# Kernel optimization log

Hardware: AMD Instinct MI355X
Metric: run time of the kernel (lower is better)

Reference implementation:

```python
import jax, jax.numpy as jnp
import numpy as np
import math

B, S, CIN, H, W = 8, 8, 64, 32, 32
COUT, K = 128, 3
PW = COUT * CIN * K * K  # 73728
P = PW + COUT            # 73856


def setup_inputs() -> dict:
    key = jax.random.key(0)
    ks = jax.random.split(key, 6)
    return {
        "x": jax.random.normal(ks[0], (B, S, CIN, H, W), dtype=jnp.float32),
        "e": jax.random.normal(ks[1], (S, P), dtype=jnp.float32),
        "mu_w": jax.random.normal(ks[2], (PW,), dtype=jnp.float32) * 0.02,
        "rho_w": jax.random.normal(ks[3], (PW,), dtype=jnp.float32) * 0.5,
        "mu_b": jax.random.normal(ks[4], (COUT,), dtype=jnp.float32) * 0.02,
        "rho_b": jax.random.normal(ks[5], (COUT,), dtype=jnp.float32) * 0.5,
    }


def _unit_log_mfg(v):
    # v: [s_n, D]; -log(2*pi)*D/2 - sum(v**2)/2  (scalar, matching torch code)
    two_pi = jnp.asarray(2.0 * math.pi, v.dtype)
    return -jnp.log(two_pi) * (v.shape[1] / 2.0) - jnp.sum(v * v) / 2.0


def reference(x, e, mu_w, rho_w, mu_b, rho_b):
    s_n = e.shape[0]
    cout = mu_b.shape[0]
    cin = x.shape[2]
    k = int(round(math.sqrt(mu_w.shape[0] / (cout * cin))))
    pw = mu_w.shape[0]

    sig_w = jax.nn.softplus(rho_w)  # log(1+exp(rho))
    sig_b = jax.nn.softplus(rho_b)
    w = mu_w[None, :] + sig_w[None, :] * e[:, :pw]          # [s_n, PW]
    b = mu_b[None, :] + sig_b[None, :] * e[:, pw:pw + cout]  # [s_n, COUT]

    entropy_q = jnp.sum(jnp.log(sig_w)) + jnp.sum(jnp.log(sig_b))
    cross_entropy_qp = _unit_log_mfg(w) + _unit_log_mfg(b)
    kl_qp = -entropy_q - cross_entropy_qp

    w5 = w.reshape(s_n, cout, cin, k, k)  # per-sample OIHW kernels

    # per-sample conv: vmap over the sample axis j; batch conv over data axis i
    def conv_one(xj, wj):  # xj [B,CIN,H,W], wj [COUT,CIN,K,K]
        return jax.lax.conv(xj, wj, (1, 1), 'VALID')

    out = jax.vmap(conv_one, in_axes=(1, 0), out_axes=1)(x, w5)  # [B,S,COUT,H',W']
    out = out + b[None, :, :, None, None]
    return out, kl_qp
```

## Files before the change

kernel.cpp:

```cpp
#include <hip/hip_runtime.h>
#include <hip/hip_bf16.h>
#include <math.h>

#define Bn    8
#define Sn    8
#define COUTc 128
#define PWc   73728
#define Pc    73856
#define WOc   30
#define NPIX  900
#define GPIX  7200
#define NSTEP 9
#define TILE  128
#define NT2   57

typedef __bf16 bf16;
typedef bf16  bf16x8 __attribute__((ext_vector_type(8)));
typedef float f32x16 __attribute__((ext_vector_type(16)));

__device__ __forceinline__ float softplus_f(float x) {
    return fmaxf(x, 0.f) + log1pf(expf(-fabsf(x)));
}

__device__ __forceinline__ unsigned int pack2(float a, float b) {
    unsigned short ua = __builtin_bit_cast(unsigned short, (bf16)a);
    unsigned short ub = __builtin_bit_cast(unsigned short, (bf16)b);
    return ((unsigned int)ub << 16) | (unsigned int)ua;
}

__device__ __forceinline__ void gl16(const void* g, void* l) {
    typedef __attribute__((address_space(1))) void gvoid;
    typedef __attribute__((address_space(3))) void lvoid;
    __builtin_amdgcn_global_load_lds((gvoid*)g, (lvoid*)l, 16, 0, 0);
}

__global__ __launch_bounds__(256) void prep_all(
        const float* __restrict__ xg, const float* __restrict__ e,
        const float* __restrict__ mu_w, const float* __restrict__ rho_w,
        const float* __restrict__ mu_b, const float* __restrict__ rho_b,
        bf16* __restrict__ xt, bf16* __restrict__ wimg,
        float* __restrict__ bq, float* __restrict__ slots) {
    const int bid = blockIdx.x;
    const int t   = threadIdx.x;

    if (bid < 512) {
        const int img  = bid >> 3;
        const int part = bid & 7;
        const int p    = part * 128 + (t >> 1);
        const int half = t & 1;
        const float* src = xg + ((size_t)img << 16) + (size_t)(half * 32) * 1024 + p;
        bf16*        dst = xt + ((size_t)img << 16) + (size_t)p * 64 + half * 32;
        #pragma unroll
        for (int o = 0; o < 4; ++o) {
            uint4 pk;
            pk.x = pack2(src[(o * 8 + 0) * 1024], src[(o * 8 + 1) * 1024]);
            pk.y = pack2(src[(o * 8 + 2) * 1024], src[(o * 8 + 3) * 1024]);
            pk.z = pack2(src[(o * 8 + 4) * 1024], src[(o * 8 + 5) * 1024]);
            pk.w = pack2(src[(o * 8 + 6) * 1024], src[(o * 8 + 7) * 1024]);
            *reinterpret_cast<uint4*>(dst + o * 8) = pk;
        }
        return;
    }

    float ls = 0.f, sq = 0.f;
    if (bid < 544) {
        const int gidx = (bid - 512) * 256 + t;
        const int co   = gidx >> 6;
        const int ci   = gidx & 63;
        const int p0   = co * 576 + ci * 9;
        float mu[9], sg[9];
        #pragma unroll
        for (int r = 0; r < 9; ++r) {
            mu[r] = mu_w[p0 + r];
            sg[r] = softplus_f(rho_w[p0 + r]);
            ls   += logf(sg[r]);
        }
        const int dstp = (co << 6) + (((ci >> 3) ^ (co & 7)) << 3) + (ci & 7);
        #pragma unroll
        for (int s = 0; s < Sn; ++s) {
            const float* es = e + s * Pc + p0;
            #pragma unroll
            for (int r = 0; r < 9; ++r) {
                float wv = fmaf(sg[r], es[r], mu[r]);
                wimg[((s * NSTEP + r) << 13) + dstp] = (bf16)wv;
                sq += wv * wv;
            }
        }
    } else {
        if (t < COUTc) {
            float sig = softplus_f(rho_b[t]);
            ls = logf(sig);
            float mu = mu_b[t];
            #pragma unroll
            for (int s = 0; s < Sn; ++s) {
                float bv = fmaf(sig, e[s * Pc + PWc + t], mu);
                bq[s * COUTc + t] = bv;
                sq += bv * bv;
            }
        }
    }

    #pragma unroll
    for (int off = 32; off > 0; off >>= 1) {
        ls += __shfl_down(ls, off);
        sq += __shfl_down(sq, off);
    }
    __shared__ float sls[4], ssq[4];
    const int lane = t & 63, wd = t >> 6;
    if (lane == 0) { sls[wd] = ls; ssq[wd] = sq; }
    __syncthreads();
    if (t == 0) {
        slots[2 * (bid - 512)]     = sls[0] + sls[1] + sls[2] + sls[3];
        slots[2 * (bid - 512) + 1] = ssq[0] + ssq[1] + ssq[2] + ssq[3];
    }
}

__global__ __launch_bounds__(128) void conv_mfma(
        const bf16* __restrict__ xt, const bf16* __restrict__ wimg,
        const float* __restrict__ bq, const float* __restrict__ slots,
        float* __restrict__ out, float* __restrict__ klout) {
    const int bid  = blockIdx.x;
    const int s    = bid & 7;
    const int tile = bid >> 3;
    const int t    = threadIdx.x;
    const int lane = t & 63;
    const int w    = t >> 6;

    __shared__ bf16 Wbuf[2][8192];
    __shared__ bf16 Xbuf[2][8192];

    const char* wsrcL = (const char*)wimg + ((size_t)(s * NSTEP) << 14)
                      + (w << 13) + (lane << 4);

    const char* xs[8];
    #pragma unroll
    for (int q = 0; q < 8; ++q) {
        int pix = w * 64 + q * 8 + (lane >> 3);
        int g   = tile * TILE + pix;
        if (g >= GPIX) g = GPIX - 1;
        int b2 = g / NPIX;
        int rr = g - b2 * NPIX;
        int oy = rr / WOc;
        int ox = rr - oy * WOc;
        int m  = (lane & 7) ^ (pix & 7);
        xs[q] = (const char*)xt
            + ((((size_t)(b2 * Sn + s) << 10) + oy * 32 + ox) << 7) + (m << 4);
    }

    f32x16 acc[2][4];
    #pragma unroll
    for (int i = 0; i < 2; ++i)
        #pragma unroll
        for (int j = 0; j < 4; ++j)
            #pragma unroll
            for (int k = 0; k < 16; ++k)
                acc[i][j][k] = 0.f;

    #define STAGE(stepc, b)                                                  \
    {                                                                        \
        const char* ws_ = wsrcL + ((stepc) << 14);                           \
        char* wl_ = (char*)(&Wbuf[(b)][0]) + (w << 13);                      \
        _Pragma("unroll")                                                    \
        for (int q = 0; q < 8; ++q)                                          \
            gl16(ws_ + (q << 10), wl_ + (q << 10));                          \
        const int roff_ = (((stepc) / 3) * 32 + ((stepc) % 3)) * 128;        \
        char* xl_ = (char*)(&Xbuf[(b)][0]) + (w << 13);                      \
        _Pragma("unroll")                                                    \
        for (int q = 0; q < 8; ++q)                                          \
            gl16(xs[q] + roff_, xl_ + (q << 10));                            \
    }

    #define COMPUTE(b)                                                       \
    {                                                                        \
        const bf16* Wl_ = &Wbuf[(b)][0];                                     \
        const bf16* Xl_ = &Xbuf[(b)][0];                                     \
        _Pragma("unroll")                                                    \
        for (int kc = 0; kc < 4; ++kc) {                                     \
            const int oct_ = ((kc << 1) + (lane >> 5)) ^ (lane & 7);         \
            bf16x8 a0 = *reinterpret_cast<const bf16x8*>(                    \
                Wl_ + ((w * 64 + (lane & 31)) << 6) + (oct_ << 3));          \
            bf16x8 a1 = *reinterpret_cast<const bf16x8*>(                    \
                Wl_ + ((w * 64 + 32 + (lane & 31)) << 6) + (oct_ << 3));     \
            bf16x8 b0 = *reinterpret_cast<const bf16x8*>(                    \
                Xl_ + (((lane & 31)) << 6) + (oct_ << 3));                   \
            bf16x8 b1 = *reinterpret_cast<const bf16x8*>(                    \
                Xl_ + ((32 + (lane & 31)) << 6) + (oct_ << 3));              \
            bf16x8 b2 = *reinterpret_cast<const bf16x8*>(                    \
                Xl_ + ((64 + (lane & 31)) << 6) + (oct_ << 3));              \
            bf16x8 b3 = *reinterpret_cast<const bf16x8*>(                    \
                Xl_ + ((96 + (lane & 31)) << 6) + (oct_ << 3));              \
            acc[0][0] = __builtin_amdgcn_mfma_f32_32x32x16_bf16(a0, b0, acc[0][0], 0, 0, 0); \
            acc[0][1] = __builtin_amdgcn_mfma_f32_32x32x16_bf16(a0, b1, acc[0][1], 0, 0, 0); \
            acc[0][2] = __builtin_amdgcn_mfma_f32_32x32x16_bf16(a0, b2, acc[0][2], 0, 0, 0); \
            acc[0][3] = __builtin_amdgcn_mfma_f32_32x32x16_bf16(a0, b3, acc[0][3], 0, 0, 0); \
            acc[1][0] = __builtin_amdgcn_mfma_f32_32x32x16_bf16(a1, b0, acc[1][0], 0, 0, 0); \
            acc[1][1] = __builtin_amdgcn_mfma_f32_32x32x16_bf16(a1, b1, acc[1][1], 0, 0, 0); \
            acc[1][2] = __builtin_amdgcn_mfma_f32_32x32x16_bf16(a1, b2, acc[1][2], 0, 0, 0); \
            acc[1][3] = __builtin_amdgcn_mfma_f32_32x32x16_bf16(a1, b3, acc[1][3], 0, 0, 0); \
        }                                                                    \
    }

    STAGE(0, 0);
    STAGE(1, 1);

    #define ITER(tt, b)                                                      \
        asm volatile("s_waitcnt vmcnt(16)" ::: "memory");                    \
        __builtin_amdgcn_s_barrier();                                        \
        __builtin_amdgcn_sched_barrier(0);                                   \
        COMPUTE(b);                                                          \
        __builtin_amdgcn_sched_barrier(0);                                   \
        __builtin_amdgcn_s_barrier();                                        \
        STAGE((tt) + 2, b);

    ITER(0, 0)
    ITER(1, 1)
    ITER(2, 0)
    ITER(3, 1)
    ITER(4, 0)
    ITER(5, 1)
    ITER(6, 0)
    asm volatile("s_waitcnt vmcnt(16)" ::: "memory");
    __builtin_amdgcn_s_barrier();
    __builtin_amdgcn_sched_barrier(0);
    COMPUTE(1);
    asm volatile("s_waitcnt vmcnt(0)" ::: "memory");
    __builtin_amdgcn_s_barrier();
    __builtin_amdgcn_sched_barrier(0);
    COMPUTE(0);

    #undef ITER
    #undef COMPUTE
    #undef STAGE

    const int colp = lane & 31;
    const int hi   = lane >> 5;
    #pragma unroll
    for (int i = 0; i < 2; ++i) {
        float bs[16];
        #pragma unroll
        for (int reg = 0; reg < 16; ++reg) {
            int co = w * 64 + i * 32 + (reg & 3) + 8 * (reg >> 2) + 4 * hi;
            bs[reg] = bq[s * COUTc + co];
        }
        #pragma unroll
        for (int j = 0; j < 4; ++j) {
            int gg = tile * TILE + j * 32 + colp;
            if (gg >= GPIX) continue;
            int b2 = gg / NPIX;
            int r2 = gg - b2 * NPIX;
            float* ob = out + (size_t)(b2 * Sn + s) * (COUTc * NPIX) + r2;
            #pragma unroll
            for (int reg = 0; reg < 16; ++reg) {
                int co = w * 64 + i * 32 + (reg & 3) + 8 * (reg >> 2) + 4 * hi;
                ob[co * NPIX] = acc[i][j][reg] + bs[reg];
            }
        }
    }

    if (bid == 0 && w == 0) {
        float ls = 0.f, sq = 0.f;
        for (int i = lane; i < 33; i += 64) {
            ls += slots[2 * i];
            sq += slots[2 * i + 1];
        }
        #pragma unroll
        for (int off = 32; off > 0; off >>= 1) {
            ls += __shfl_down(ls, off);
            sq += __shfl_down(sq, off);
        }
        if (lane == 0)
            *klout = -ls + 0.91893853320467274f * (float)Pc + 0.5f * sq;
    }
}

extern "C" void kernel_launch(void* const* d_in, const int* in_sizes, int n_in,
                              void* d_out, int out_size, void* d_ws, size_t ws_size,
                              hipStream_t stream) {
    const float* x     = (const float*)d_in[0];
    const float* e     = (const float*)d_in[1];
    const float* mu_w  = (const float*)d_in[2];
    const float* rho_w = (const float*)d_in[3];
    const float* mu_b  = (const float*)d_in[4];
    const float* rho_b = (const float*)d_in[5];
    float* out = (float*)d_out;

    bf16*  wimg  = (bf16*)d_ws;
    float* bq    = (float*)((char*)d_ws + 1179648);
    float* slots = (float*)((char*)d_ws + 1183744);
    bf16*  xt    = (bf16*)((char*)d_ws + 1187840);

    prep_all<<<dim3(545), dim3(256), 0, stream>>>(
        x, e, mu_w, rho_w, mu_b, rho_b, xt, wimg, bq, slots);

    conv_mfma<<<dim3(NT2 * Sn), dim3(128), 0, stream>>>(
        xt, wimg, bq, slots, out, out + (out_size - 1));
}
```

Measured before the change: 35.17 us.

## Replace LDS-staged MFMA conv with direct-global-load single-wave tiles

Drops the double-buffered LDS staging with global_load_lds and barriers. Instead, each 64-thread block computes a 64-cout by 64-pixel tile and loads MFMA operands straight from global memory into registers. The weight and activation workspace layouts are changed to channel-octet-major so each lane's 16-byte fragment is read directly. Running many more small blocks (1808) is meant to raise occupancy and remove sync overhead, at the cost of less data reuse per block and more L2 traffic.

Measured after the change: 40.98 us. 16.5% more time.

```diff
diff --git a/kernel.cpp b/kernel.cpp
--- a/kernel.cpp
+++ b/kernel.cpp
@@ -11,8 +11,6 @@
 #define NPIX  900
 #define GPIX  7200
 #define NSTEP 9
-#define TILE  128
-#define NT2   57
 
 typedef __bf16 bf16;
 typedef bf16  bf16x8 __attribute__((ext_vector_type(8)));
@@ -28,17 +26,11 @@
     return ((unsigned int)ub << 16) | (unsigned int)ua;
 }
 
-__device__ __forceinline__ void gl16(const void* g, void* l) {
-    typedef __attribute__((address_space(1))) void gvoid;
-    typedef __attribute__((address_space(3))) void lvoid;
-    __builtin_amdgcn_global_load_lds((gvoid*)g, (lvoid*)l, 16, 0, 0);
-}
-
 __global__ __launch_bounds__(256) void prep_all(
         const float* __restrict__ xg, const float* __restrict__ e,
         const float* __restrict__ mu_w, const float* __restrict__ rho_w,
         const float* __restrict__ mu_b, const float* __restrict__ rho_b,
-        bf16* __restrict__ xt, bf16* __restrict__ wimg,
+        bf16* __restrict__ xt, bf16* __restrict__ wq,
         float* __restrict__ bq, float* __restrict__ slots) {
     const int bid = blockIdx.x;
     const int t   = threadIdx.x;
@@ -46,10 +38,9 @@
     if (bid < 512) {
         const int img  = bid >> 3;
         const int part = bid & 7;
-        const int p    = part * 128 + (t >> 1);
-        const int half = t & 1;
+        const int p    = part * 128 + (t & 127);
+        const int half = t >> 7;
         const float* src = xg + ((size_t)img << 16) + (size_t)(half * 32) * 1024 + p;
-        bf16*        dst = xt + ((size_t)img << 16) + (size_t)p * 64 + half * 32;
         #pragma unroll
         for (int o = 0; o < 4; ++o) {
             uint4 pk;
@@ -57,7 +48,8 @@
             pk.y = pack2(src[(o * 8 + 2) * 1024], src[(o * 8 + 3) * 1024]);
             pk.z = pack2(src[(o * 8 + 4) * 1024], src[(o * 8 + 5) * 1024]);
             pk.w = pack2(src[(o * 8 + 6) * 1024], src[(o * 8 + 7) * 1024]);
-            *reinterpret_cast<uint4*>(dst + o * 8) = pk;
+            size_t idx16 = ((size_t)(img * 8 + half * 4 + o) << 10) + p;
+            *reinterpret_cast<uint4*>(xt + (idx16 << 3)) = pk;
         }
         return;
     }
@@ -75,14 +67,14 @@
             sg[r] = softplus_f(rho_w[p0 + r]);
             ls   += logf(sg[r]);
         }
-        const int dstp = (co << 6) + (((ci >> 3) ^ (co & 7)) << 3) + (ci & 7);
+        const int dstp = ((((ci >> 3) << 7) + co) << 3) + (ci & 7);
         #pragma unroll
         for (int s = 0; s < Sn; ++s) {
             const float* es = e + s * Pc + p0;
             #pragma unroll
             for (int r = 0; r < 9; ++r) {
                 float wv = fmaf(sg[r], es[r], mu[r]);
-                wimg[((s * NSTEP + r) << 13) + dstp] = (bf16)wv;
+                wq[(((s * NSTEP + r) << 10) << 3) + dstp] = (bf16)wv;
                 sq += wv * wv;
             }
         }
@@ -115,161 +107,89 @@
     }
 }
 
-__global__ __launch_bounds__(128) void conv_mfma(
-        const bf16* __restrict__ xt, const bf16* __restrict__ wimg,
+__global__ __launch_bounds__(64) void conv_mfma(
+        const bf16* __restrict__ xt, const bf16* __restrict__ wq,
         const float* __restrict__ bq, const float* __restrict__ slots,
         float* __restrict__ out, float* __restrict__ klout) {
     const int bid  = blockIdx.x;
     const int s    = bid & 7;
-    const int tile = bid >> 3;
-    const int t    = threadIdx.x;
-    const int lane = t & 63;
-    const int w    = t >> 6;
-
-    __shared__ bf16 Wbuf[2][8192];
-    __shared__ bf16 Xbuf[2][8192];
-
-    const char* wsrcL = (const char*)wimg + ((size_t)(s * NSTEP) << 14)
-                      + (w << 13) + (lane << 4);
-
-    const char* xs[8];
-    #pragma unroll
-    for (int q = 0; q < 8; ++q) {
-        int pix = w * 64 + q * 8 + (lane >> 3);
-        int g   = tile * TILE + pix;
-        if (g >= GPIX) g = GPIX - 1;
-        int b2 = g / NPIX;
-        int rr = g - b2 * NPIX;
-        int oy = rr / WOc;
-        int ox = rr - oy * WOc;
-        int m  = (lane & 7) ^ (pix & 7);
-        xs[q] = (const char*)xt
-            + ((((size_t)(b2 * Sn + s) << 10) + oy * 32 + ox) << 7) + (m << 4);
-    }
-
-    f32x16 acc[2][4];
-    #pragma unroll
-    for (int i = 0; i < 2; ++i)
-        #pragma unroll
-        for (int j = 0; j < 4; ++j)
-            #pragma unroll
-            for (int k = 0; k < 16; ++k)
-                acc[i][j][k] = 0.f;
-
-    #define STAGE(stepc, b)                                                  \
-    {                                                                        \
-        const char* ws_ = wsrcL + ((stepc) << 14);                           \
-        char* wl_ = (char*)(&Wbuf[(b)][0]) + (w << 13);                      \
-        _Pragma("unroll")                                                    \
-        for (int q = 0; q < 8; ++q)                                          \
-            gl16(ws_ + (q << 10), wl_ + (q << 10));                          \
-        const int roff_ = (((stepc) / 3) * 32 + ((stepc) % 3)) * 128;        \
-        char* xl_ = (char*)(&Xbuf[(b)][0]) + (w << 13);                      \
-        _Pragma("unroll")                                                    \
-        for (int q = 0; q < 8; ++q)                                          \
-            gl16(xs[q] + roff_, xl_ + (q << 10));                            \
-    }
-
-    #define COMPUTE(b)                                                       \
-    {                                                                        \
-        const bf16* Wl_ = &Wbuf[(b)][0];                                     \
-        const bf16* Xl_ = &Xbuf[(b)][0];                                     \
-        _Pragma("unroll")                                                    \
-        for (int kc = 0; kc < 4; ++kc) {                                     \
-            const int oct_ = ((kc << 1) + (lane >> 5)) ^ (lane & 7);         \
-            bf16x8 a0 = *reinterpret_cast<const bf16x8*>(                    \
-                Wl_ + ((w * 64 + (lane & 31)) << 6) + (oct_ << 3));          \
-            bf16x8 a1 = *reinterpret_cast<const bf16x8*>(                    \
-                Wl_ + ((w * 64 + 32 + (lane & 31)) << 6) + (oct_ << 3));     \
-            bf16x8 b0 = *reinterpret_cast<const bf16x8*>(                    \
-                Xl_ + (((lane & 31)) << 6) + (oct_ << 3));                   \
-            bf16x8 b1 = *reinterpret_cast<const bf16x8*>(                    \
-                Xl_ + ((32 + (lane & 31)) << 6) + (oct_ << 3));              \
-            bf16x8 b2 = *reinterpret_cast<const bf16x8*>(                    \
-                Xl_ + ((64 + (lane & 31)) << 6) + (oct_ << 3));              \
-            bf16x8 b3 = *reinterpret_cast<const bf16x8*>(                    \
-                Xl_ + ((96 + (lane & 31)) << 6) + (oct_ << 3));              \
-            acc[0][0] = __builtin_amdgcn_mfma_f32_32x32x16_bf16(a0, b0, acc[0][0], 0, 0, 0); \
-            acc[0][1] = __builtin_amdgcn_mfma_f32_32x32x16_bf16(a0, b1, acc[0][1], 0, 0, 0); \
-            acc[0][2] = __builtin_amdgcn_mfma_f32_32x32x16_bf16(a0, b2, acc[0][2], 0, 0, 0); \
-            acc[0][3] = __builtin_amdgcn_mfma_f32_32x32x16_bf16(a0, b3, acc[0][3], 0, 0, 0); \
-            acc[1][0] = __builtin_amdgcn_mfma_f32_32x32x16_bf16(a1, b0, acc[1][0], 0, 0, 0); \
-            acc[1][1] = __builtin_amdgcn_mfma_f32_32x32x16_bf16(a1, b1, acc[1][1], 0, 0, 0); \
-            acc[1][2] = __builtin_amdgcn_mfma_f32_32x32x16_bf16(a1, b2, acc[1][2], 0, 0, 0); \
-            acc[1][3] = __builtin_amdgcn_mfma_f32_32x32x16_bf16(a1, b3, acc[1][3], 0, 0, 0); \
-        }                                                                    \
-    }
-
-    STAGE(0, 0);
-    STAGE(1, 1);
-
-    #define ITER(tt, b)                                                      \
-        asm volatile("s_waitcnt vmcnt(16)" ::: "memory");                    \
-        __builtin_amdgcn_s_barrier();                                        \
-        __builtin_amdgcn_sched_barrier(0);                                   \
-        COMPUTE(b);                                                          \
-        __builtin_amdgcn_sched_barrier(0);                                   \
-        __builtin_amdgcn_s_barrier();                                        \
-        STAGE((tt) + 2, b);
-
-    ITER(0, 0)
-    ITER(1, 1)
-    ITER(2, 0)
-    ITER(3, 1)
-    ITER(4, 0)
-    ITER(5, 1)
-    ITER(6, 0)
-    asm volatile("s_waitcnt vmcnt(16)" ::: "memory");
-    __builtin_amdgcn_s_barrier();
-    __builtin_amdgcn_sched_barrier(0);
-    COMPUTE(1);
-    asm volatile("s_waitcnt vmcnt(0)" ::: "memory");
-    __builtin_amdgcn_s_barrier();
-    __builtin_amdgcn_sched_barrier(0);
-    COMPUTE(0);
-
-    #undef ITER
-    #undef COMPUTE
-    #undef STAGE
-
-    const int colp = lane & 31;
+    const int idx  = bid >> 3;
+    const int coh  = idx & 1;
+    const int pt   = idx >> 1;
+    const int lane = threadIdx.x;
     const int hi   = lane >> 5;
+    const int lo   = lane & 31;
+
+    const bf16* wp = wq + ((((size_t)(s * NSTEP) << 10) + hi * 128 + coh * 64 + lo) << 3);
+
+    const bf16 *xp0, *xp1;
+    int g0, g1;
+    {
+        int g = pt * 64 + lo;         g0 = g; if (g > GPIX - 1) g = GPIX - 1;
+        int b2 = g / NPIX, rr = g - b2 * NPIX, oy = rr / WOc, ox = rr - oy * WOc;
+        xp0 = xt + ((((size_t)((b2 * Sn + s) * 8 + hi) << 10) + oy * 32 + ox) << 3);
+        g = pt * 64 + 32 + lo;        g1 = g; if (g > GPIX - 1) g = GPIX - 1;
+        b2 = g / NPIX; rr = g - b2 * NPIX; oy = rr / WOc; ox = rr - oy * WOc;
+        xp1 = xt + ((((size_t)((b2 * Sn + s) * 8 + hi) << 10) + oy * 32 + ox) << 3);
+    }
+
+    f32x16 acc00, acc01, acc10, acc11;
+    #pragma unroll
+    for (int k = 0; k < 16; ++k) { acc00[k] = 0.f; acc01[k] = 0.f; acc10[k] = 0.f; acc11[k] = 0.f; }
+
+    #pragma unroll
+    for (int r = 0; r < NSTEP; ++r) {
+        const int dyx = (r / 3) * 32 + (r % 3);
+        #pragma unroll
+        for (int kc = 0; kc < 4; ++kc) {
+            bf16x8 a0 = *reinterpret_cast<const bf16x8*>(wp + (((r << 10) + kc * 256) << 3));
+            bf16x8 a1 = *reinterpret_cast<const bf16x8*>(wp + (((r << 10) + kc * 256 + 32) << 3));
+            bf16x8 b0 = *reinterpret_cast<const bf16x8*>(xp0 + ((kc * 2048 + dyx) << 3));
+            bf16x8 b1 = *reinterpret_cast<const bf16x8*>(xp1 + ((kc * 2048 + dyx) << 3));
+            acc00 = __builtin_amdgcn_mfma_f32_32x32x16_bf16(a0, b0, acc00, 0, 0, 0);
+            acc01 = __builtin_amdgcn_mfma_f32_32x32x16_bf16(a0, b1, acc01, 0, 0, 0);
+            acc10 = __builtin_amdgcn_mfma_f32_32x32x16_bf16(a1, b0, acc10, 0, 0, 0);
+            acc11 = __builtin_amdgcn_mfma_f32_32x32x16_bf16(a1, b1, acc11, 0, 0, 0);
+        }
+    }
+
     #pragma unroll
     for (int i = 0; i < 2; ++i) {
+        const f32x16& aj0 = i ? acc10 : acc00;
+        const f32x16& aj1 = i ? acc11 : acc01;
         float bs[16];
         #pragma unroll
         for (int reg = 0; reg < 16; ++reg) {
-            int co = w * 64 + i * 32 + (reg & 3) + 8 * (reg >> 2) + 4 * hi;
+            int co = coh * 64 + i * 32 + (reg & 3) + 8 * (reg >> 2) + 4 * hi;
             bs[reg] = bq[s * COUTc + co];
         }
-        #pragma unroll
-        for (int j = 0; j < 4; ++j) {
-            int gg = tile * TILE + j * 32 + colp;
-            if (gg >= GPIX) continue;
-            int b2 = gg / NPIX;
-            int r2 = gg - b2 * NPIX;
+        if (g0 < GPIX) {
+            int b2 = g0 / NPIX, r2 = g0 - b2 * NPIX;
             float* ob = out + (size_t)(b2 * Sn + s) * (COUTc * NPIX) + r2;
             #pragma unroll
             for (int reg = 0; reg < 16; ++reg) {
-                int co = w * 64 + i * 32 + (reg & 3) + 8 * (reg >> 2) + 4 * hi;
-                ob[co * NPIX] = acc[i][j][reg] + bs[reg];
-            }
-        }
-    }
-
-    if (bid == 0 && w == 0) {
+                int co = coh * 64 + i * 32 + (reg & 3) + 8 * (reg >> 2) + 4 * hi;
+                ob[co * NPIX] = aj0[reg] + bs[reg];
+            }
+        }
+        if (g1 < GPIX) {
+            int b2 = g1 / NPIX, r2 = g1 - b2 * NPIX;
+            float* ob = out + (size_t)(b2 * Sn + s) * (COUTc * NPIX) + r2;
+            #pragma unroll
+            for (int reg = 0; reg < 16; ++reg) {
+                int co = coh * 64 + i * 32 + (reg & 3) + 8 * (reg >> 2) + 4 * hi;
+                ob[co * NPIX] = aj1[reg] + bs[reg];
+            }
+        }
+    }
+
+    if (bid == 0 && lane == 0) {
         float ls = 0.f, sq = 0.f;
-        for (int i = lane; i < 33; i += 64) {
-            ls += slots[2 * i];
-            sq += slots[2 * i + 1];
-        }
-        #pragma unroll
-        for (int off = 32; off > 0; off >>= 1) {
-            ls += __shfl_down(ls, off);
-            sq += __shfl_down(sq, off);
-        }
-        if (lane == 0)
-            *klout = -ls + 0.91893853320467274f * (float)Pc + 0.5f * sq;
+        for (int i2 = 0; i2 < 33; ++i2) {
+            ls += slots[2 * i2];
+            sq += slots[2 * i2 + 1];
+        }
+        *klout = -ls + 0.91893853320467274f * (float)Pc + 0.5f * sq;
     }
 }
 
@@ -284,14 +204,14 @@
     const float* rho_b = (const float*)d_in[5];
     float* out = (float*)d_out;
 
-    bf16*  wimg  = (bf16*)d_ws;
+    bf16*  wq    = (bf16*)d_ws;
     float* bq    = (float*)((char*)d_ws + 1179648);
     float* slots = (float*)((char*)d_ws + 1183744);
     bf16*  xt    = (bf16*)((char*)d_ws + 1187840);
 
     prep_all<<<dim3(545), dim3(256), 0, stream>>>(
-        x, e, mu_w, rho_w, mu_b, rho_b, xt, wimg, bq, slots);
-
-    conv_mfma<<<dim3(NT2 * Sn), dim3(128), 0, stream>>>(
-        xt, wimg, bq, slots, out, out + (out_size - 1));
-}
+        x, e, mu_w, rho_w, mu_b, rho_b, xt, wq, bq, slots);
+
+    conv_mfma<<<dim3(1808), dim3(64), 0, stream>>>(
+        xt, wq, bq, slots, out, out + (out_size - 1));
+}
```
